# Performance work log

Hardware: AMD Instinct MI355X
Metric: run time of the kernel (lower is better)

Reference implementation:

```python
import jax, jax.numpy as jnp
import numpy as np

LN_EPS = 1e-5

def _layernorm(x, gamma, beta):
    mu = jnp.mean(x, axis=-1, keepdims=True)
    var = jnp.mean(jnp.square(x - mu), axis=-1, keepdims=True)
    return (x - mu) * jax.lax.rsqrt(var + LN_EPS) * gamma + beta

def _gcn_layer(A_hat, H, W, b, g, beta):
    # batched dense-equivalent of per-batch torch.sparse.mm: (B,N,N)@(B,N,F)
    H = jnp.einsum('bnm,bmf->bnf', A_hat, H)
    H = H @ W + b            # Linear
    H = _layernorm(H, g, beta)
    return jax.nn.relu(H)    # dropout is identity in eval

def setup_inputs() -> dict:
    key = jax.random.key(0)
    ks = jax.random.split(key, 8)
    B, N, F, Hd, K, G = 16, 2048, 64, 256, 128, 18
    fuse = Hd + G  # 274
    return {
        'A_hat': jax.random.uniform(ks[0], (B, N, N), dtype=jnp.float32),
        'X': jax.random.normal(ks[1], (B, N, F), dtype=jnp.float32),
        'global_vec': jax.random.normal(ks[2], (B, G), dtype=jnp.float32),
        'W1': jax.random.normal(ks[3], (F, Hd), dtype=jnp.float32) / np.sqrt(F),
        'b1': jnp.zeros((Hd,), jnp.float32),
        'g1': jnp.ones((Hd,), jnp.float32),
        'beta1': jnp.zeros((Hd,), jnp.float32),
        'W2': jax.random.normal(ks[4], (Hd, Hd), dtype=jnp.float32) / np.sqrt(Hd),
        'b2': jnp.zeros((Hd,), jnp.float32),
        'g2': jnp.ones((Hd,), jnp.float32),
        'beta2': jnp.zeros((Hd,), jnp.float32),
        'Ws': jax.random.normal(ks[5], (fuse, 1), dtype=jnp.float32) / np.sqrt(fuse),
        'bs': jnp.zeros((1,), jnp.float32),
        'Wa': jax.random.normal(ks[6], (fuse, K), dtype=jnp.float32) / np.sqrt(fuse),
        'ba': jnp.zeros((K,), jnp.float32),
    }

def reference(A_hat, X, global_vec, W1, b1, g1, beta1, W2, b2, g2, beta2, Ws, bs, Wa, ba):
    H = _gcn_layer(A_hat, X, W1, b1, g1, beta1)
    H = _gcn_layer(A_hat, H, W2, b2, g2, beta2)
    gcnout = jnp.mean(H, axis=1)                       # 'mean' readout -> (B, hidden)
    fused = jnp.concatenate([gcnout, global_vec], axis=-1)  # (B, hidden+18)
    pred_y_reg = (fused @ Ws + bs)[:, 0]               # (B,)
    pred_arr_reg = fused @ Wa + ba                     # (B, K)
    return pred_y_reg, pred_arr_reg
```

## Files before the change

kernel.cpp:

```cpp
#include <hip/hip_runtime.h>

typedef unsigned short u16;
typedef __attribute__((ext_vector_type(8))) short bf16x8;
typedef __attribute__((ext_vector_type(16))) float f32x16;

__device__ __forceinline__ unsigned f2bf(float f) {
  unsigned u = __float_as_uint(f);
  return (u + 0x7fffu + ((u >> 16) & 1u)) >> 16;
}

__device__ __forceinline__ void async16(const u16* g, u16* l) {
  __builtin_amdgcn_global_load_lds(
      (const __attribute__((address_space(1))) void*)g,
      (__attribute__((address_space(3))) void*)l, 16, 0, 0);
}

template<int EPI>
__global__ __launch_bounds__(256, 2) void mm64(
    const u16* __restrict__ Aop, const u16* __restrict__ Bop,
    int K, int lda, int ldb, int ldc,
    long long sA, long long sB, long long sC,
    const float* __restrict__ bias, const float* __restrict__ gam,
    const float* __restrict__ bet, u16* __restrict__ Cb, float* __restrict__ gcn)
{
  __shared__ __align__(16) u16 As[2][64 * 64];
  __shared__ __align__(16) u16 Bs[256 * 64];
  const int tid = threadIdx.x;
  const int w = tid >> 6, lane = tid & 63, l31 = lane & 31, half = lane >> 5;
  const int m0 = blockIdx.x * 64, n0 = blockIdx.y * 256, bz = blockIdx.z;

  const int srow = tid >> 3;
  const int clog = (tid & 7) ^ (srow & 7);
  const u16* Ag = Aop + sA * bz + (size_t)(m0 + srow) * lda + clog * 8;
  const u16* Bg = Bop + sB * bz + (size_t)(n0 + srow) * ldb + clog * 8;

  f32x16 acc[2][2];
#pragma unroll
  for (int i = 0; i < 2; i++)
#pragma unroll
    for (int j = 0; j < 2; j++)
#pragma unroll
      for (int r = 0; r < 16; r++) acc[i][j][r] = 0.f;

  const int niter = K >> 6;
  async16(Ag, As[0] + tid * 8);
  async16(Ag + (size_t)32 * lda, As[0] + 2048 + tid * 8);

  for (int i = 0; i < niter; i++) {
    const int k0 = i << 6;
    __syncthreads();
#pragma unroll
    for (int p = 0; p < 8; p++)
      async16(Bg + (size_t)p * 32 * ldb + k0, Bs + p * 2048 + tid * 8);
    if (i + 1 < niter) {
      u16* dst = As[(i + 1) & 1];
      async16(Ag + k0 + 64, dst + tid * 8);
      async16(Ag + (size_t)32 * lda + k0 + 64, dst + 2048 + tid * 8);
      __builtin_amdgcn_s_waitcnt(0x0F72);
    } else {
      __builtin_amdgcn_s_waitcnt(0x0F70);
    }
    __builtin_amdgcn_s_barrier();
    __asm__ volatile("" ::: "memory");
    const u16* Ab = As[i & 1];
#pragma unroll
    for (int kk = 0; kk < 4; kk++) {
      const int pc = ((kk * 2 + half) ^ (l31 & 7)) * 8;
      const bf16x8 a0 = *(const bf16x8*)(Ab + l31 * 64 + pc);
      const bf16x8 a1 = *(const bf16x8*)(Ab + (32 + l31) * 64 + pc);
      const int nr = (w * 64 + l31) * 64;
      const bf16x8 b0 = *(const bf16x8*)(Bs + nr + pc);
      const bf16x8 b1 = *(const bf16x8*)(Bs + nr + 32 * 64 + pc);
      acc[0][0] = __builtin_amdgcn_mfma_f32_32x32x16_bf16(a0, b0, acc[0][0], 0, 0, 0);
      acc[0][1] = __builtin_amdgcn_mfma_f32_32x32x16_bf16(a0, b1, acc[0][1], 0, 0, 0);
      acc[1][0] = __builtin_amdgcn_mfma_f32_32x32x16_bf16(a1, b0, acc[1][0], 0, 0, 0);
      acc[1][1] = __builtin_amdgcn_mfma_f32_32x32x16_bf16(a1, b1, acc[1][1], 0, 0, 0);
    }
  }

  __syncthreads();
  const int col0 = w * 64 + l31;

  if constexpr (EPI == 0) {
#pragma unroll
    for (int mt = 0; mt < 2; mt++)
#pragma unroll
      for (int r = 0; r < 16; r++) {
        const int rl = (r & 3) + 8 * (r >> 2) + 4 * half;
        const long long row = (long long)m0 + mt * 32 + rl;
        Cb[sC * bz + row * ldc + n0 + col0]      = (u16)f2bf(acc[mt][0][r]);
        Cb[sC * bz + row * ldc + n0 + col0 + 32] = (u16)f2bf(acc[mt][1][r]);
      }
    return;
  }

  const float b0 = bias[col0], b1 = bias[col0 + 32];
  float s2[2][16];
#pragma unroll
  for (int mt = 0; mt < 2; mt++)
#pragma unroll
    for (int r = 0; r < 16; r++) {
      acc[mt][0][r] += b0;
      acc[mt][1][r] += b1;
      s2[mt][r] = acc[mt][0][r] + acc[mt][1][r];
    }
#pragma unroll
  for (int off = 1; off <= 16; off <<= 1)
#pragma unroll
    for (int mt = 0; mt < 2; mt++)
#pragma unroll
      for (int r = 0; r < 16; r++) s2[mt][r] += __shfl_xor(s2[mt][r], off);

  float* sm = (float*)Bs;
  if (l31 == 0) {
#pragma unroll
    for (int mt = 0; mt < 2; mt++)
#pragma unroll
      for (int r = 0; r < 16; r++) {
        const int rl = (r & 3) + 8 * (r >> 2) + 4 * half;
        sm[w * 64 + mt * 32 + rl] = s2[mt][r];
      }
  }
  __syncthreads();
  if (tid < 64)
    sm[256 + tid] = (sm[tid] + sm[64 + tid] + sm[128 + tid] + sm[192 + tid]) * (1.f / 256.f);
  __syncthreads();
  float4 mu4[2][4];
#pragma unroll
  for (int mt = 0; mt < 2; mt++)
#pragma unroll
    for (int g = 0; g < 4; g++)
      mu4[mt][g] = *(const float4*)(sm + 256 + mt * 32 + g * 8 + 4 * half);

  float q2[2][16];
#pragma unroll
  for (int mt = 0; mt < 2; mt++)
#pragma unroll
    for (int r = 0; r < 16; r++) {
      const float mu = ((const float*)&mu4[mt][r >> 2])[r & 3];
      const float d0 = acc[mt][0][r] - mu, d1 = acc[mt][1][r] - mu;
      q2[mt][r] = d0 * d0 + d1 * d1;
    }
#pragma unroll
  for (int off = 1; off <= 16; off <<= 1)
#pragma unroll
    for (int mt = 0; mt < 2; mt++)
#pragma unroll
      for (int r = 0; r < 16; r++) q2[mt][r] += __shfl_xor(q2[mt][r], off);
  __syncthreads();
  if (l31 == 0) {
#pragma unroll
    for (int mt = 0; mt < 2; mt++)
#pragma unroll
      for (int r = 0; r < 16; r++) {
        const int rl = (r & 3) + 8 * (r >> 2) + 4 * half;
        sm[w * 64 + mt * 32 + rl] = q2[mt][r];
      }
  }
  __syncthreads();
  if (tid < 64)
    sm[320 + tid] = rsqrtf(
        (sm[tid] + sm[64 + tid] + sm[128 + tid] + sm[192 + tid]) * (1.f / 256.f) + 1e-5f);
  __syncthreads();
  float4 iv4[2][4];
#pragma unroll
  for (int mt = 0; mt < 2; mt++)
#pragma unroll
    for (int g = 0; g < 4; g++)
      iv4[mt][g] = *(const float4*)(sm + 320 + mt * 32 + g * 8 + 4 * half);

  const float g0 = gam[col0], g1 = gam[col0 + 32];
  const float e0 = bet[col0], e1 = bet[col0 + 32];
  if constexpr (EPI == 1) {
#pragma unroll
    for (int mt = 0; mt < 2; mt++)
#pragma unroll
      for (int r = 0; r < 16; r++) {
        const float mu = ((const float*)&mu4[mt][r >> 2])[r & 3];
        const float iv = ((const float*)&iv4[mt][r >> 2])[r & 3];
        const int rl = (r & 3) + 8 * (r >> 2) + 4 * half;
        const long long row = (long long)m0 + mt * 32 + rl;
        const float y0 = fmaxf((acc[mt][0][r] - mu) * iv * g0 + e0, 0.f);
        const float y1 = fmaxf((acc[mt][1][r] - mu) * iv * g1 + e1, 0.f);
        Cb[sC * bz + row * ldc + col0]      = (u16)f2bf(y0);
        Cb[sC * bz + row * ldc + col0 + 32] = (u16)f2bf(y1);
      }
  } else {
    float c0 = 0.f, c1 = 0.f;
#pragma unroll
    for (int mt = 0; mt < 2; mt++)
#pragma unroll
      for (int r = 0; r < 16; r++) {
        const float mu = ((const float*)&mu4[mt][r >> 2])[r & 3];
        const float iv = ((const float*)&iv4[mt][r >> 2])[r & 3];
        c0 += fmaxf((acc[mt][0][r] - mu) * iv * g0 + e0, 0.f);
        c1 += fmaxf((acc[mt][1][r] - mu) * iv * g1 + e1, 0.f);
      }
    c0 += __shfl_xor(c0, 32);
    c1 += __shfl_xor(c1, 32);
    if (half == 0) {
      atomicAdd(gcn + bz * 256 + col0, c0);
      atomicAdd(gcn + bz * 256 + col0 + 32, c1);
    }
  }
}

__global__ __launch_bounds__(256) void convert_bf16(const float* __restrict__ in,
                                                    u16* __restrict__ out, long long n8)
{
  const long long i = (long long)blockIdx.x * 256 + threadIdx.x;
  if (i >= n8) return;
  const float4 a = ((const float4*)in)[2 * i];
  const float4 b = ((const float4*)in)[2 * i + 1];
  uint4 r;
  r.x = f2bf(a.x) | (f2bf(a.y) << 16);
  r.y = f2bf(a.z) | (f2bf(a.w) << 16);
  r.z = f2bf(b.x) | (f2bf(b.y) << 16);
  r.w = f2bf(b.z) | (f2bf(b.w) << 16);
  ((uint4*)out)[i] = r;
}

__global__ __launch_bounds__(256) void transpose_bf16(const float* __restrict__ in,
                                                      u16* __restrict__ outp,
                                                      int rows, int cols)
{
  const int n = rows * cols;
  const int o = blockIdx.x * 256 + threadIdx.x;
  if (o < n) {
    const int c = o / rows, r = o - c * rows;
    outp[o] = (u16)f2bf(in[r * cols + c]);
  }
}

__global__ void zero_kernel(float* p, int n) {
  const int i = blockIdx.x * 256 + threadIdx.x;
  if (i < n) p[i] = 0.f;
}

__global__ __launch_bounds__(128) void final_kernel(
    const float* __restrict__ gcn, const float* __restrict__ gv,
    const float* __restrict__ Ws, const float* __restrict__ bs,
    const float* __restrict__ Wa, const float* __restrict__ ba,
    float* __restrict__ out)
{
  const int b = blockIdx.x, t = threadIdx.x;
  __shared__ float fused[274];
  fused[t] = gcn[b * 256 + t] * (1.f / 2048.f);
  fused[128 + t] = gcn[b * 256 + 128 + t] * (1.f / 2048.f);
  if (t < 18) fused[256 + t] = gv[b * 18 + t];
  __syncthreads();
  float acc = ba[t];
  for (int i = 0; i < 274; i++) acc = fmaf(fused[i], Wa[i * 128 + t], acc);
  out[16 + b * 128 + t] = acc;
  if (t < 64) {
    float p = 0.f;
    for (int i = t; i < 274; i += 64) p += fused[i] * Ws[i];
#pragma unroll
    for (int off = 32; off >= 1; off >>= 1) p += __shfl_xor(p, off);
    if (t == 0) out[b] = p + bs[0];
  }
}

extern "C" void kernel_launch(void* const* d_in, const int* in_sizes, int n_in,
                              void* d_out, int out_size, void* d_ws, size_t ws_size,
                              hipStream_t stream)
{
  const float* A   = (const float*)d_in[0];
  const float* X   = (const float*)d_in[1];
  const float* GV  = (const float*)d_in[2];
  const float* W1  = (const float*)d_in[3];
  const float* b1  = (const float*)d_in[4];
  const float* g1  = (const float*)d_in[5];
  const float* be1 = (const float*)d_in[6];
  const float* W2  = (const float*)d_in[7];
  const float* b2  = (const float*)d_in[8];
  const float* g2  = (const float*)d_in[9];
  const float* be2 = (const float*)d_in[10];
  const float* Ws  = (const float*)d_in[11];
  const float* bs  = (const float*)d_in[12];
  const float* Wa  = (const float*)d_in[13];
  const float* ba  = (const float*)d_in[14];
  float* out = (float*)d_out;
  (void)in_sizes; (void)n_in; (void)out_size; (void)ws_size;

  char* ws = (char*)d_ws;
  u16*   Abf = (u16*)(ws + 0);
  u16*   Xbf = (u16*)(ws + 134217728);
  u16*   W1T = (u16*)(ws + 138412032);
  u16*   W2T = (u16*)(ws + 138444800);
  u16*   XWT = (u16*)(ws + 138575872);
  u16*   H1  = (u16*)(ws + 155353088);
  u16*   HWT = (u16*)(ws + 172130304);
  float* GCN = (float*)(ws + 188907520);

  zero_kernel<<<16, 256, 0, stream>>>(GCN, 4096);
  convert_bf16<<<1024, 256, 0, stream>>>(X, Xbf, 262144LL);
  transpose_bf16<<<64, 256, 0, stream>>>(W1, W1T, 64, 256);
  transpose_bf16<<<256, 256, 0, stream>>>(W2, W2T, 256, 256);
  convert_bf16<<<32768, 256, 0, stream>>>(A, Abf, 8388608LL);

  mm64<0><<<dim3(4, 8, 16), 256, 0, stream>>>(
      W1T, Xbf, 64, 64, 64, 2048, 0LL, 131072LL, 524288LL,
      nullptr, nullptr, nullptr, XWT, nullptr);

  mm64<1><<<dim3(32, 1, 16), 256, 0, stream>>>(
      Abf, XWT, 2048, 2048, 2048, 256, 4194304LL, 524288LL, 524288LL,
      b1, g1, be1, H1, nullptr);

  mm64<0><<<dim3(4, 8, 16), 256, 0, stream>>>(
      W2T, H1, 256, 256, 256, 2048, 0LL, 524288LL, 524288LL,
      nullptr, nullptr, nullptr, HWT, nullptr);

  mm64<2><<<dim3(32, 1, 16), 256, 0, stream>>>(
      Abf, HWT, 2048, 2048, 2048, 256, 4194304LL, 524288LL, 524288LL,
      b2, g2, be2, nullptr, GCN);

  final_kernel<<<16, 128, 0, stream>>>(GCN, GV, Ws, bs, Wa, ba, out);
}
```

Before: 600.5 us.

## Enlarge GEMM tile to 128x256 with 8 waves, double-buffered B, and batch-interleaved block order

Replaces the 64x256 tile kernel with a 128x256 tile run by 512 threads in a 2x4 wave grid. Both A and B tiles are now double-buffered and prefetched one k-step ahead, so B loads no longer stall each iteration. Block indices are remapped so consecutive blocks span different batches, which changes L2 locality. The larger tile halves the number of times the B operand is re-read, but it needs more LDS (96KB per block) and leaves fewer blocks per launch, which can hurt occupancy.

```diff
diff --git a/kernel.cpp b/kernel.cpp
--- a/kernel.cpp
+++ b/kernel.cpp
@@ -16,18 +16,26 @@
 }
 
 template<int EPI>
-__global__ __launch_bounds__(256, 2) void mm64(
+__global__ __launch_bounds__(512, 2) void mm128(
     const u16* __restrict__ Aop, const u16* __restrict__ Bop,
     int K, int lda, int ldb, int ldc,
     long long sA, long long sB, long long sC,
     const float* __restrict__ bias, const float* __restrict__ gam,
     const float* __restrict__ bet, u16* __restrict__ Cb, float* __restrict__ gcn)
 {
-  __shared__ __align__(16) u16 As[2][64 * 64];
-  __shared__ __align__(16) u16 Bs[256 * 64];
+  __shared__ __align__(16) u16 As[2][128 * 64];
+  __shared__ __align__(16) u16 Bs[2][256 * 64];
   const int tid = threadIdx.x;
   const int w = tid >> 6, lane = tid & 63, l31 = lane & 31, half = lane >> 5;
-  const int m0 = blockIdx.x * 64, n0 = blockIdx.y * 256, bz = blockIdx.z;
+  const int wm = w >> 2, wn = w & 3;
+
+  const int fid = blockIdx.x + gridDim.x * (blockIdx.y + gridDim.y * blockIdx.z);
+  const int pb = gridDim.x * gridDim.y;
+  int idx = fid >> 3;
+  int bz = fid & 7;
+  if (idx >= pb) { bz += 8; idx -= pb; }
+  const int m0 = (int)(idx % gridDim.x) * 128;
+  const int n0 = (int)(idx / gridDim.x) * 256;
 
   const int srow = tid >> 3;
   const int clog = (tid & 7) ^ (srow & 7);
@@ -43,43 +51,49 @@
       for (int r = 0; r < 16; r++) acc[i][j][r] = 0.f;
 
   const int niter = K >> 6;
-  async16(Ag, As[0] + tid * 8);
-  async16(Ag + (size_t)32 * lda, As[0] + 2048 + tid * 8);
+  {
+    u16* Ad = As[0]; u16* Bd = Bs[0];
+    async16(Ag, Ad + tid * 8);
+    async16(Ag + (size_t)64 * lda, Ad + 4096 + tid * 8);
+#pragma unroll
+    for (int p = 0; p < 4; p++)
+      async16(Bg + (size_t)(p * 64) * ldb, Bd + p * 4096 + tid * 8);
+  }
 
   for (int i = 0; i < niter; i++) {
-    const int k0 = i << 6;
-    __syncthreads();
-#pragma unroll
-    for (int p = 0; p < 8; p++)
-      async16(Bg + (size_t)p * 32 * ldb + k0, Bs + p * 2048 + tid * 8);
     if (i + 1 < niter) {
-      u16* dst = As[(i + 1) & 1];
-      async16(Ag + k0 + 64, dst + tid * 8);
-      async16(Ag + (size_t)32 * lda + k0 + 64, dst + 2048 + tid * 8);
-      __builtin_amdgcn_s_waitcnt(0x0F72);
+      const int k1 = (i + 1) << 6;
+      u16* Ad = As[(i + 1) & 1]; u16* Bd = Bs[(i + 1) & 1];
+      async16(Ag + k1, Ad + tid * 8);
+      async16(Ag + (size_t)64 * lda + k1, Ad + 4096 + tid * 8);
+#pragma unroll
+      for (int p = 0; p < 4; p++)
+        async16(Bg + (size_t)(p * 64) * ldb + k1, Bd + p * 4096 + tid * 8);
+      __builtin_amdgcn_s_waitcnt(0x0F76);
     } else {
       __builtin_amdgcn_s_waitcnt(0x0F70);
     }
     __builtin_amdgcn_s_barrier();
     __asm__ volatile("" ::: "memory");
     const u16* Ab = As[i & 1];
+    const u16* Bb = Bs[i & 1];
 #pragma unroll
     for (int kk = 0; kk < 4; kk++) {
       const int pc = ((kk * 2 + half) ^ (l31 & 7)) * 8;
-      const bf16x8 a0 = *(const bf16x8*)(Ab + l31 * 64 + pc);
-      const bf16x8 a1 = *(const bf16x8*)(Ab + (32 + l31) * 64 + pc);
-      const int nr = (w * 64 + l31) * 64;
-      const bf16x8 b0 = *(const bf16x8*)(Bs + nr + pc);
-      const bf16x8 b1 = *(const bf16x8*)(Bs + nr + 32 * 64 + pc);
+      const bf16x8 a0 = *(const bf16x8*)(Ab + (wm * 64 + l31) * 64 + pc);
+      const bf16x8 a1 = *(const bf16x8*)(Ab + (wm * 64 + 32 + l31) * 64 + pc);
+      const bf16x8 b0 = *(const bf16x8*)(Bb + (wn * 64 + l31) * 64 + pc);
+      const bf16x8 b1 = *(const bf16x8*)(Bb + (wn * 64 + 32 + l31) * 64 + pc);
       acc[0][0] = __builtin_amdgcn_mfma_f32_32x32x16_bf16(a0, b0, acc[0][0], 0, 0, 0);
       acc[0][1] = __builtin_amdgcn_mfma_f32_32x32x16_bf16(a0, b1, acc[0][1], 0, 0, 0);
       acc[1][0] = __builtin_amdgcn_mfma_f32_32x32x16_bf16(a1, b0, acc[1][0], 0, 0, 0);
       acc[1][1] = __builtin_amdgcn_mfma_f32_32x32x16_bf16(a1, b1, acc[1][1], 0, 0, 0);
     }
-  }
-
-  __syncthreads();
-  const int col0 = w * 64 + l31;
+    __asm__ volatile("" ::: "memory");
+    __builtin_amdgcn_s_barrier();
+  }
+
+  const int col0 = wn * 64 + l31;
 
   if constexpr (EPI == 0) {
 #pragma unroll
@@ -87,21 +101,22 @@
 #pragma unroll
       for (int r = 0; r < 16; r++) {
         const int rl = (r & 3) + 8 * (r >> 2) + 4 * half;
-        const long long row = (long long)m0 + mt * 32 + rl;
+        const long long row = (long long)m0 + wm * 64 + mt * 32 + rl;
         Cb[sC * bz + row * ldc + n0 + col0]      = (u16)f2bf(acc[mt][0][r]);
         Cb[sC * bz + row * ldc + n0 + col0 + 32] = (u16)f2bf(acc[mt][1][r]);
       }
     return;
   }
 
-  const float b0 = bias[col0], b1 = bias[col0 + 32];
+  __syncthreads();
+  const float bia0 = bias[col0], bia1 = bias[col0 + 32];
   float s2[2][16];
 #pragma unroll
   for (int mt = 0; mt < 2; mt++)
 #pragma unroll
     for (int r = 0; r < 16; r++) {
-      acc[mt][0][r] += b0;
-      acc[mt][1][r] += b1;
+      acc[mt][0][r] += bia0;
+      acc[mt][1][r] += bia1;
       s2[mt][r] = acc[mt][0][r] + acc[mt][1][r];
     }
 #pragma unroll
@@ -111,26 +126,26 @@
 #pragma unroll
       for (int r = 0; r < 16; r++) s2[mt][r] += __shfl_xor(s2[mt][r], off);
 
-  float* sm = (float*)Bs;
+  float* sm = (float*)As;
   if (l31 == 0) {
 #pragma unroll
     for (int mt = 0; mt < 2; mt++)
 #pragma unroll
       for (int r = 0; r < 16; r++) {
         const int rl = (r & 3) + 8 * (r >> 2) + 4 * half;
-        sm[w * 64 + mt * 32 + rl] = s2[mt][r];
-      }
-  }
-  __syncthreads();
-  if (tid < 64)
-    sm[256 + tid] = (sm[tid] + sm[64 + tid] + sm[128 + tid] + sm[192 + tid]) * (1.f / 256.f);
+        sm[wn * 128 + wm * 64 + mt * 32 + rl] = s2[mt][r];
+      }
+  }
+  __syncthreads();
+  if (tid < 128)
+    sm[512 + tid] = (sm[tid] + sm[128 + tid] + sm[256 + tid] + sm[384 + tid]) * (1.f / 256.f);
   __syncthreads();
   float4 mu4[2][4];
 #pragma unroll
   for (int mt = 0; mt < 2; mt++)
 #pragma unroll
     for (int g = 0; g < 4; g++)
-      mu4[mt][g] = *(const float4*)(sm + 256 + mt * 32 + g * 8 + 4 * half);
+      mu4[mt][g] = *(const float4*)(sm + 512 + wm * 64 + mt * 32 + g * 8 + 4 * half);
 
   float q2[2][16];
 #pragma unroll
@@ -154,20 +169,20 @@
 #pragma unroll
       for (int r = 0; r < 16; r++) {
         const int rl = (r & 3) + 8 * (r >> 2) + 4 * half;
-        sm[w * 64 + mt * 32 + rl] = q2[mt][r];
-      }
-  }
-  __syncthreads();
-  if (tid < 64)
-    sm[320 + tid] = rsqrtf(
-        (sm[tid] + sm[64 + tid] + sm[128 + tid] + sm[192 + tid]) * (1.f / 256.f) + 1e-5f);
+        sm[wn * 128 + wm * 64 + mt * 32 + rl] = q2[mt][r];
+      }
+  }
+  __syncthreads();
+  if (tid < 128)
+    sm[640 + tid] = rsqrtf(
+        (sm[tid] + sm[128 + tid] + sm[256 + tid] + sm[384 + tid]) * (1.f / 256.f) + 1e-5f);
   __syncthreads();
   float4 iv4[2][4];
 #pragma unroll
   for (int mt = 0; mt < 2; mt++)
 #pragma unroll
     for (int g = 0; g < 4; g++)
-      iv4[mt][g] = *(const float4*)(sm + 320 + mt * 32 + g * 8 + 4 * half);
+      iv4[mt][g] = *(const float4*)(sm + 640 + wm * 64 + mt * 32 + g * 8 + 4 * half);
 
   const float g0 = gam[col0], g1 = gam[col0 + 32];
   const float e0 = bet[col0], e1 = bet[col0 + 32];
@@ -179,7 +194,7 @@
         const float mu = ((const float*)&mu4[mt][r >> 2])[r & 3];
         const float iv = ((const float*)&iv4[mt][r >> 2])[r & 3];
         const int rl = (r & 3) + 8 * (r >> 2) + 4 * half;
-        const long long row = (long long)m0 + mt * 32 + rl;
+        const long long row = (long long)m0 + wm * 64 + mt * 32 + rl;
         const float y0 = fmaxf((acc[mt][0][r] - mu) * iv * g0 + e0, 0.f);
         const float y1 = fmaxf((acc[mt][1][r] - mu) * iv * g1 + e1, 0.f);
         Cb[sC * bz + row * ldc + col0]      = (u16)f2bf(y0);
@@ -299,19 +314,19 @@
   transpose_bf16<<<256, 256, 0, stream>>>(W2, W2T, 256, 256);
   convert_bf16<<<32768, 256, 0, stream>>>(A, Abf, 8388608LL);
 
-  mm64<0><<<dim3(4, 8, 16), 256, 0, stream>>>(
+  mm128<0><<<dim3(2, 8, 16), 512, 0, stream>>>(
       W1T, Xbf, 64, 64, 64, 2048, 0LL, 131072LL, 524288LL,
       nullptr, nullptr, nullptr, XWT, nullptr);
 
-  mm64<1><<<dim3(32, 1, 16), 256, 0, stream>>>(
+  mm128<1><<<dim3(16, 1, 16), 512, 0, stream>>>(
       Abf, XWT, 2048, 2048, 2048, 256, 4194304LL, 524288LL, 524288LL,
       b1, g1, be1, H1, nullptr);
 
-  mm64<0><<<dim3(4, 8, 16), 256, 0, stream>>>(
+  mm128<0><<<dim3(2, 8, 16), 512, 0, stream>>>(
       W2T, H1, 256, 256, 256, 2048, 0LL, 524288LL, 524288LL,
       nullptr, nullptr, nullptr, HWT, nullptr);
 
-  mm64<2><<<dim3(32, 1, 16), 256, 0, stream>>>(
+  mm128<2><<<dim3(16, 1, 16), 512, 0, stream>>>(
       Abf, HWT, 2048, 2048, 2048, 256, 4194304LL, 524288LL, 524288LL,
       b2, g2, be2, nullptr, GCN);
 
```

Measured after the change: 600.1 us. No clear change (-0.1%).
